# Performance work log

Hardware: AMD Instinct MI355X
Metric: run time of the kernel (lower is better)

## Reference

```python
import jax, jax.numpy as jnp
import numpy as np

N = 100000      # nodes
E = 1600000     # directed edges (avg degree 16)
F_IN = 256      # dataset.num_node_features
HID = 64        # hidden
C = 40          # dataset.num_classes


def setup_inputs() -> dict:
    key = jax.random.key(0)
    k0, k1, k2, k3 = jax.random.split(key, 4)
    x = jax.random.normal(k0, (N, F_IN), dtype=jnp.float32)
    edge_index = jax.random.randint(k1, (2, E), 0, N, dtype=jnp.int32)
    # Glorot-style init like GCNConv.reset_parameters
    W1 = jax.random.normal(k2, (F_IN, HID), dtype=jnp.float32) * (1.0 / np.sqrt(F_IN))
    b1 = jnp.zeros((HID,), dtype=jnp.float32)
    W2 = jax.random.normal(k3, (HID, C), dtype=jnp.float32) * (1.0 / np.sqrt(HID))
    b2 = jnp.zeros((C,), dtype=jnp.float32)
    return {"x": x, "edge_index": edge_index, "W1": W1, "b1": b1, "W2": W2, "b2": b2}


def gcn_conv(x, row, col, norm, W, b):
    # PyG GCNConv: out[col] += norm * (x @ W)[row]; then + bias
    n = x.shape[0]
    h = x @ W                                   # [N, out]
    msg = h[row] * norm[:, None]                # [E+N, out] gather + scale
    out = jax.ops.segment_sum(msg, col, num_segments=n)  # scatter-add
    return out + b


def _norm_coeffs(edge_index, n, dtype):
    # add self-loops, then symmetric normalization D^{-1/2} A D^{-1/2}
    loop = jnp.arange(n, dtype=edge_index.dtype)
    row = jnp.concatenate([edge_index[0], loop])
    col = jnp.concatenate([edge_index[1], loop])
    deg = jax.ops.segment_sum(jnp.ones_like(col, dtype=dtype), col, num_segments=n)
    dis = jnp.where(deg > 0, jax.lax.rsqrt(jnp.maximum(deg, 1.0)), 0.0)
    return row, col, dis[row] * dis[col]


def reference(x, edge_index, W1, b1, W2, b2):
    n = x.shape[0]
    row, col, norm = _norm_coeffs(edge_index, n, x.dtype)
    h = jax.nn.relu(gcn_conv(x, row, col, norm, W1, b1))
    # F.dropout(p=0.5, training=False) is identity in eval mode
    out = gcn_conv(h, row, col, norm, W2, b2)
    return jax.nn.log_softmax(out, axis=1)
```

## Files before the change

kernel.cpp:

```cpp
#include <hip/hip_runtime.h>
#include <math.h>

#define N_NODES 100000
#define N_EDGES 1600000
#define F_INDIM 256
#define HID 64
#define NCLS 40
#define NBKT 196
#define BKT_CAP 10240
#define EPB 8192

typedef __attribute__((ext_vector_type(8))) short short8;
typedef __attribute__((ext_vector_type(4))) float floatx4;

__device__ __forceinline__ unsigned short f2bf(float f) {
  unsigned u = __float_as_uint(f);
  unsigned r = (u + 0x7FFFu + ((u >> 16) & 1u)) >> 16;
  return (unsigned short)r;
}
__device__ __forceinline__ float bf2f(unsigned short h) {
  return __uint_as_float(((unsigned)h) << 16);
}
__device__ __forceinline__ void add8(float* a, uint4 u) {
  a[0] += __uint_as_float(u.x << 16);
  a[1] += __uint_as_float(u.x & 0xFFFF0000u);
  a[2] += __uint_as_float(u.y << 16);
  a[3] += __uint_as_float(u.y & 0xFFFF0000u);
  a[4] += __uint_as_float(u.z << 16);
  a[5] += __uint_as_float(u.z & 0xFFFF0000u);
  a[6] += __uint_as_float(u.w << 16);
  a[7] += __uint_as_float(u.w & 0xFFFF0000u);
}


__global__ __launch_bounds__(256) void k_zero(int* __restrict__ gcur,
                                              int* __restrict__ start) {
  int t = threadIdx.x;
  if (t < NBKT) gcur[t] = 0;
  if (t == 0) start[N_NODES] = N_EDGES;
}


__global__ __launch_bounds__(256) void k_binA(const int* __restrict__ row,
                                              const int* __restrict__ col,
                                              int* __restrict__ gcur,
                                              unsigned int* __restrict__ bktdata) {
  __shared__ int hist[NBKT];
  __shared__ int cur[NBKT];
  __shared__ int gbase[NBKT];
  const int t = threadIdx.x;
  const int e0 = blockIdx.x * EPB;
  const int n = min(EPB, N_EDGES - e0);
  if (t < NBKT) hist[t] = 0;
  __syncthreads();
  for (int i = t; i < n; i += 256) atomicAdd(&hist[col[e0 + i] >> 9], 1);
  __syncthreads();
  if (t < NBKT) {
    cur[t] = 0;
    int h = hist[t];
    gbase[t] = (h > 0) ? atomicAdd(&gcur[t], h) : 0;
  }
  __syncthreads();
  for (int i = t; i < n; i += 256) {
    int c = col[e0 + i];
    int r = row[e0 + i];
    int b = c >> 9;
    int p = atomicAdd(&cur[b], 1);
    bktdata[(size_t)b * BKT_CAP + gbase[b] + p] =
        ((unsigned)(c & 511) << 17) | (unsigned)r;
  }
}


__global__ __launch_bounds__(256) void k_histdis(const int* __restrict__ gcur,
                                                 const unsigned int* __restrict__ bktdata,
                                                 int* __restrict__ lscan,
                                                 float* __restrict__ dis) {
  __shared__ int h[512];
  const int b = blockIdx.x, t = threadIdx.x;
  h[t] = 0; h[t + 256] = 0;
  __syncthreads();
  const int cnt = gcur[b];
  const unsigned int* p = bktdata + (size_t)b * BKT_CAP;
  for (int i = t; i < cnt; i += 256) atomicAdd(&h[p[i] >> 17], 1);
  __syncthreads();
  const int n0 = b * 512 + t, n1 = n0 + 256;
  const int c0 = h[t], c1 = h[t + 256];
  if (n0 < N_NODES) dis[n0] = rsqrtf((float)(c0 + 1));
  if (n1 < N_NODES) dis[n1] = rsqrtf((float)(c1 + 1));
#pragma unroll
  for (int off = 1; off < 512; off <<= 1) {
    int u0 = (t >= off) ? h[t - off] : 0;
    int u1 = ((t + 256) >= off) ? h[t + 256 - off] : 0;
    __syncthreads();
    h[t] += u0; h[t + 256] += u1;
    __syncthreads();
  }
  if (n0 < N_NODES) lscan[n0] = h[t] - c0;
  if (n1 < N_NODES) lscan[n1] = h[t + 256] - c1;
}


__global__ __launch_bounds__(256) void k_scan2(const int* __restrict__ gcur,
                                               int* __restrict__ bsumS) {
  __shared__ int s[256];
  const int t = threadIdx.x;
  int v = (t < NBKT) ? gcur[t] : 0;
  s[t] = v;
  __syncthreads();
#pragma unroll
  for (int off = 1; off < 256; off <<= 1) {
    int u = (t >= off) ? s[t - off] : 0;
    __syncthreads();
    s[t] += u;
    __syncthreads();
  }
  if (t < NBKT) bsumS[t] = s[t] - v;
}


__global__ __launch_bounds__(256) void k_place(const int* __restrict__ gcur,
                                               const unsigned int* __restrict__ bktdata,
                                               const int* __restrict__ lscan,
                                               const int* __restrict__ bsumS,
                                               int* __restrict__ start,
                                               int* __restrict__ esrc) {
  __shared__ int cur[512];
  __shared__ int sbase[512];
  const int b = blockIdx.x, t = threadIdx.x;
  const int base = bsumS[b];
  const int n0 = b * 512 + t, n1 = n0 + 256;
  int s0 = ((n0 < N_NODES) ? lscan[n0] : 0) + base;
  int s1 = ((n1 < N_NODES) ? lscan[n1] : 0) + base;
  sbase[t] = s0; sbase[t + 256] = s1;
  if (n0 < N_NODES) start[n0] = s0;
  if (n1 < N_NODES) start[n1] = s1;
  cur[t] = 0; cur[t + 256] = 0;
  __syncthreads();
  const int cnt = gcur[b];
  const unsigned int* p = bktdata + (size_t)b * BKT_CAP;
  for (int i = t; i < cnt; i += 256) {
    unsigned u = p[i];
    int ld = u >> 17;
    int src = u & 0x1FFFF;
    int pos = sbase[ld] + atomicAdd(&cur[ld], 1);
    esrc[pos] = src;
  }
}


#define KP 264

__global__ __launch_bounds__(256) void k_gemm1(const float* __restrict__ x,
                                               const float* __restrict__ W1,
                                               const float* __restrict__ dis,
                                               unsigned short* __restrict__ h1b) {
  __shared__ unsigned short wt[HID * KP];
  const int tid = threadIdx.x;
  const int lane = tid & 63;
  const int w = tid >> 6;
  const int quad = lane >> 4;
  const int l15 = lane & 15;
  const int rowBase = blockIdx.x * 64;

#pragma unroll
  for (int i = 0; i < 16; ++i) {
    int f = tid + 256 * i;
    int k = f >> 4;
    int n0 = (f & 15) * 4;
    float4 v = *(const float4*)&W1[(size_t)k * HID + n0];
    wt[(n0 + 0) * KP + k] = f2bf(v.x);
    wt[(n0 + 1) * KP + k] = f2bf(v.y);
    wt[(n0 + 2) * KP + k] = f2bf(v.z);
    wt[(n0 + 3) * KP + k] = f2bf(v.w);
  }
  __syncthreads();

  const int ar = rowBase + w * 16 + l15;
  const float* xrow = x + (size_t)((ar < N_NODES) ? ar : N_NODES - 1) * F_INDIM + quad * 8;

  floatx4 acc[4];
#pragma unroll
  for (int c = 0; c < 4; ++c) acc[c] = (floatx4){0.f, 0.f, 0.f, 0.f};

#pragma unroll
  for (int kc = 0; kc < F_INDIM; kc += 32) {
    const float4 va = *(const float4*)(xrow + kc);
    const float4 vb = *(const float4*)(xrow + kc + 4);
    short8 a;
    a[0] = (short)f2bf(va.x); a[1] = (short)f2bf(va.y);
    a[2] = (short)f2bf(va.z); a[3] = (short)f2bf(va.w);
    a[4] = (short)f2bf(vb.x); a[5] = (short)f2bf(vb.y);
    a[6] = (short)f2bf(vb.z); a[7] = (short)f2bf(vb.w);
#pragma unroll
    for (int c = 0; c < 4; ++c) {
      const short8 b = *(const short8*)&wt[(c * 16 + l15) * KP + kc + quad * 8];
      acc[c] = __builtin_amdgcn_mfma_f32_16x16x32_bf16(a, b, acc[c], 0, 0, 0);
    }
  }

#pragma unroll
  for (int reg = 0; reg < 4; ++reg) {
    int gr = rowBase + w * 16 + quad * 4 + reg;
    if (gr < N_NODES) {
      float d = dis[gr];
#pragma unroll
      for (int c = 0; c < 4; ++c)
        h1b[(size_t)gr * HID + c * 16 + l15] = f2bf(d * acc[c][reg]);
    }
  }
}


__global__ __launch_bounds__(256) void k_agg1(const int* __restrict__ esrc,
                                              const int* __restrict__ start,
                                              const float* __restrict__ dis,
                                              const unsigned short* __restrict__ h1b,
                                              const float* __restrict__ b1,
                                              unsigned short* __restrict__ ab) {
  int gid = blockIdx.x * 256 + threadIdx.x;
  int node = gid >> 3;
  int q = gid & 7;
  if (node >= N_NODES) return;
  const uint4* hp4 = (const uint4*)h1b;
  int i = start[node];
  const int e1 = start[node + 1];
  float acc[8];
#pragma unroll
  for (int j = 0; j < 8; ++j) acc[j] = 0.f;
  for (; i + 2 <= e1; i += 2) {
    int s0 = esrc[i];
    int s1 = esrc[i + 1];
    uint4 u0 = hp4[(size_t)s0 * 8 + q];
    uint4 u1 = hp4[(size_t)s1 * 8 + q];
    add8(acc, u0);
    add8(acc, u1);
  }
  if (i < e1) {
    uint4 u = hp4[(size_t)esrc[i] * 8 + q];
    add8(acc, u);
  }
  uint4 us = hp4[(size_t)node * 8 + q];
  add8(acc, us);
  float d = dis[node];
  float4 ba = *(const float4*)&b1[q * 8];
  float4 bb = *(const float4*)&b1[q * 8 + 4];
  float v0 = fmaxf(d * acc[0] + ba.x, 0.f);
  float v1 = fmaxf(d * acc[1] + ba.y, 0.f);
  float v2 = fmaxf(d * acc[2] + ba.z, 0.f);
  float v3 = fmaxf(d * acc[3] + ba.w, 0.f);
  float v4 = fmaxf(d * acc[4] + bb.x, 0.f);
  float v5 = fmaxf(d * acc[5] + bb.y, 0.f);
  float v6 = fmaxf(d * acc[6] + bb.z, 0.f);
  float v7 = fmaxf(d * acc[7] + bb.w, 0.f);
  uint4 o;
  o.x = (unsigned)f2bf(v0) | ((unsigned)f2bf(v1) << 16);
  o.y = (unsigned)f2bf(v2) | ((unsigned)f2bf(v3) << 16);
  o.z = (unsigned)f2bf(v4) | ((unsigned)f2bf(v5) << 16);
  o.w = (unsigned)f2bf(v6) | ((unsigned)f2bf(v7) << 16);
  ((uint4*)ab)[(size_t)node * 8 + q] = o;
}


#define AP 72

__global__ __launch_bounds__(256) void k_gemm2(const unsigned short* __restrict__ ab,
                                               const float* __restrict__ W2,
                                               const float* __restrict__ dis,
                                               unsigned short* __restrict__ gb) {
  __shared__ unsigned short as[64 * AP];
  __shared__ unsigned short w2t[48 * AP];
  const int tid = threadIdx.x;
  const int lane = tid & 63;
  const int w = tid >> 6;
  const int quad = lane >> 4;
  const int l15 = lane & 15;
  const int rowBase = blockIdx.x * 64;

  for (int i = tid; i < 48 * 64; i += 256) {
    int n = i >> 6;
    int k = i & 63;
    w2t[n * AP + k] = (n < NCLS) ? f2bf(W2[(size_t)k * NCLS + n]) : (unsigned short)0;
  }
#pragma unroll
  for (int i = 0; i < 2; ++i) {
    int f = tid + 256 * i;
    int r = f >> 3;
    int q = f & 7;
    int gr = rowBase + r;
    short8 v = (short8){0, 0, 0, 0, 0, 0, 0, 0};
    if (gr < N_NODES) v = *(const short8*)&ab[(size_t)gr * HID + q * 8];
    *(short8*)&as[r * AP + q * 8] = v;
  }
  __syncthreads();

  floatx4 acc[3];
#pragma unroll
  for (int c = 0; c < 3; ++c) acc[c] = (floatx4){0.f, 0.f, 0.f, 0.f};

#pragma unroll
  for (int kh = 0; kh < 2; ++kh) {
    const short8 a = *(const short8*)&as[(w * 16 + l15) * AP + kh * 32 + quad * 8];
#pragma unroll
    for (int c = 0; c < 3; ++c) {
      const short8 b = *(const short8*)&w2t[(c * 16 + l15) * AP + kh * 32 + quad * 8];
      acc[c] = __builtin_amdgcn_mfma_f32_16x16x32_bf16(a, b, acc[c], 0, 0, 0);
    }
  }

#pragma unroll
  for (int reg = 0; reg < 4; ++reg) {
    int gr = rowBase + w * 16 + quad * 4 + reg;
    if (gr < N_NODES) {
      float d = dis[gr];
#pragma unroll
      for (int c = 0; c < 3; ++c) {
        int cc = c * 16 + l15;
        gb[(size_t)gr * 64 + cc] = f2bf(d * acc[c][reg]);
      }
      gb[(size_t)gr * 64 + 48 + l15] = 0;
    }
  }
}


__global__ __launch_bounds__(256) void k_agg2ls(const int* __restrict__ esrc,
                                                const int* __restrict__ start,
                                                const float* __restrict__ dis,
                                                const unsigned short* __restrict__ gb,
                                                const float* __restrict__ b2,
                                                float* __restrict__ out) {
  int gid = blockIdx.x * 256 + threadIdx.x;
  int node = gid >> 3;
  int q = gid & 7;
  if (node >= N_NODES) return;
  const uint4* gp4 = (const uint4*)gb;
  int i = start[node];
  const int e1 = start[node + 1];
  float acc[8];
#pragma unroll
  for (int j = 0; j < 8; ++j) acc[j] = 0.f;
  for (; i + 2 <= e1; i += 2) {
    int s0 = esrc[i];
    int s1 = esrc[i + 1];
    uint4 u0 = gp4[(size_t)s0 * 8 + q];
    uint4 u1 = gp4[(size_t)s1 * 8 + q];
    add8(acc, u0);
    add8(acc, u1);
  }
  if (i < e1) {
    uint4 u = gp4[(size_t)esrc[i] * 8 + q];
    add8(acc, u);
  }
  uint4 us = gp4[(size_t)node * 8 + q];
  add8(acc, us);
  const bool wr = q < 5;
  float v0 = 0.f, v1 = 0.f, v2 = 0.f, v3 = 0.f, v4 = 0.f, v5 = 0.f, v6 = 0.f, v7 = 0.f;
  float m = -INFINITY;
  if (wr) {
    float d = dis[node];
    float4 ba = *(const float4*)&b2[q * 8];
    float4 bb = *(const float4*)&b2[q * 8 + 4];
    v0 = d * acc[0] + ba.x;
    v1 = d * acc[1] + ba.y;
    v2 = d * acc[2] + ba.z;
    v3 = d * acc[3] + ba.w;
    v4 = d * acc[4] + bb.x;
    v5 = d * acc[5] + bb.y;
    v6 = d * acc[6] + bb.z;
    v7 = d * acc[7] + bb.w;
    m = fmaxf(fmaxf(fmaxf(v0, v1), fmaxf(v2, v3)),
              fmaxf(fmaxf(v4, v5), fmaxf(v6, v7)));
  }
#pragma unroll
  for (int off = 1; off < 8; off <<= 1) m = fmaxf(m, __shfl_xor(m, off));
  float el = 0.f;
  if (wr) {
    el = __expf(v0 - m) + __expf(v1 - m) + __expf(v2 - m) + __expf(v3 - m) +
         __expf(v4 - m) + __expf(v5 - m) + __expf(v6 - m) + __expf(v7 - m);
  }
#pragma unroll
  for (int off = 1; off < 8; off <<= 1) el += __shfl_xor(el, off);
  float ls = logf(el);
  if (wr) {
    float4 o1 = make_float4(v0 - m - ls, v1 - m - ls, v2 - m - ls, v3 - m - ls);
    float4 o2 = make_float4(v4 - m - ls, v5 - m - ls, v6 - m - ls, v7 - m - ls);
    *(float4*)&out[(size_t)node * NCLS + q * 8] = o1;
    *(float4*)&out[(size_t)node * NCLS + q * 8 + 4] = o2;
  }
}


extern "C" void kernel_launch(void* const* d_in, const int* in_sizes, int n_in,
                              void* d_out, int out_size, void* d_ws, size_t ws_size,
                              hipStream_t stream) {
  const float* x  = (const float*)d_in[0];
  const int*   ei = (const int*)d_in[1];
  const float* W1 = (const float*)d_in[2];
  const float* b1 = (const float*)d_in[3];
  const float* W2 = (const float*)d_in[4];
  const float* b2 = (const float*)d_in[5];
  float* out = (float*)d_out;

  const int* row = ei;
  const int* col = ei + N_EDGES;

  int*            esrc    = (int*)d_ws;
  unsigned int*   bktdata = (unsigned int*)(esrc + N_EDGES);
  unsigned short* h1b     = (unsigned short*)(bktdata + (size_t)NBKT * BKT_CAP);
  unsigned short* ab      = h1b + (size_t)N_NODES * HID;
  float*          dis     = (float*)(ab + (size_t)N_NODES * HID);
  int*            lscan   = (int*)(dis + N_NODES);
  int*            start   = lscan + N_NODES;
  int*            gcur    = start + N_NODES + 1;
  int*            bsumS   = gcur + NBKT;
  unsigned short* gb      = h1b;

  k_zero<<<1, 256, 0, stream>>>(gcur, start);
  k_binA<<<(N_EDGES + EPB - 1) / EPB, 256, 0, stream>>>(row, col, gcur, bktdata);
  k_histdis<<<NBKT, 256, 0, stream>>>(gcur, bktdata, lscan, dis);
  k_scan2<<<1, 256, 0, stream>>>(gcur, bsumS);
  k_place<<<NBKT, 256, 0, stream>>>(gcur, bktdata, lscan, bsumS, start, esrc);

  k_gemm1<<<(N_NODES + 63) / 64, 256, 0, stream>>>(x, W1, dis, h1b);
  k_agg1<<<(N_NODES * 8 + 255) / 256, 256, 0, stream>>>(esrc, start, dis, h1b, b1, ab);

  k_gemm2<<<(N_NODES + 63) / 64, 256, 0, stream>>>(ab, W2, dis, gb);
  k_agg2ls<<<(N_NODES * 8 + 255) / 256, 256, 0, stream>>>(esrc, start, dis, gb, b2, out);
}
```

Before: 325.2 us.

## Fuse CSR build histogram, scan and placement into one kernel; unroll gathers by four

The per-bucket histogram/dis kernel, the single-block bucket scan and the placement kernel are merged into one kernel. Each block now computes its own bucket base offset by reducing the counts of the preceding buckets with wave shuffles. This removes two launches and the lscan/bsumS round trips through global memory. Separately, both aggregation kernels unroll the neighbour gather loop from 2 to 4 to put more loads in flight, at some cost in registers.

```diff
diff --git a/kernel.cpp b/kernel.cpp
--- a/kernel.cpp
+++ b/kernel.cpp
@@ -33,11 +33,9 @@
 }
 
 
-__global__ __launch_bounds__(256) void k_zero(int* __restrict__ gcur,
-                                              int* __restrict__ start) {
+__global__ __launch_bounds__(256) void k_zero(int* __restrict__ gcur) {
   int t = threadIdx.x;
   if (t < NBKT) gcur[t] = 0;
-  if (t == 0) start[N_NODES] = N_EDGES;
 }
 
 
@@ -72,18 +70,30 @@
 }
 
 
-__global__ __launch_bounds__(256) void k_histdis(const int* __restrict__ gcur,
-                                                 const unsigned int* __restrict__ bktdata,
-                                                 int* __restrict__ lscan,
-                                                 float* __restrict__ dis) {
+__global__ __launch_bounds__(256) void k_build2(const int* __restrict__ gcur,
+                                                const unsigned int* __restrict__ bktdata,
+                                                float* __restrict__ dis,
+                                                int* __restrict__ start,
+                                                int* __restrict__ esrc) {
   __shared__ int h[512];
+  __shared__ int cur[512];
+  __shared__ int sbase[512];
+  __shared__ int wsum[4];
   const int b = blockIdx.x, t = threadIdx.x;
-  h[t] = 0; h[t + 256] = 0;
-  __syncthreads();
+  h[t] = 0; h[t + 256] = 0; cur[t] = 0; cur[t + 256] = 0;
+  int pv = (t < b) ? gcur[t] : 0;
+#pragma unroll
+  for (int off = 1; off < 64; off <<= 1) pv += __shfl_xor(pv, off);
+  if ((t & 63) == 0) wsum[t >> 6] = pv;
+  if (b == 0 && t == 0) start[N_NODES] = N_EDGES;
+  __syncthreads();
+  const int base = wsum[0] + wsum[1] + wsum[2] + wsum[3];
+
   const int cnt = gcur[b];
   const unsigned int* p = bktdata + (size_t)b * BKT_CAP;
   for (int i = t; i < cnt; i += 256) atomicAdd(&h[p[i] >> 17], 1);
   __syncthreads();
+
   const int n0 = b * 512 + t, n1 = n0 + 256;
   const int c0 = h[t], c1 = h[t + 256];
   if (n0 < N_NODES) dis[n0] = rsqrtf((float)(c0 + 1));
@@ -96,49 +106,13 @@
     h[t] += u0; h[t + 256] += u1;
     __syncthreads();
   }
-  if (n0 < N_NODES) lscan[n0] = h[t] - c0;
-  if (n1 < N_NODES) lscan[n1] = h[t + 256] - c1;
-}
-
-
-__global__ __launch_bounds__(256) void k_scan2(const int* __restrict__ gcur,
-                                               int* __restrict__ bsumS) {
-  __shared__ int s[256];
-  const int t = threadIdx.x;
-  int v = (t < NBKT) ? gcur[t] : 0;
-  s[t] = v;
-  __syncthreads();
-#pragma unroll
-  for (int off = 1; off < 256; off <<= 1) {
-    int u = (t >= off) ? s[t - off] : 0;
-    __syncthreads();
-    s[t] += u;
-    __syncthreads();
-  }
-  if (t < NBKT) bsumS[t] = s[t] - v;
-}
-
-
-__global__ __launch_bounds__(256) void k_place(const int* __restrict__ gcur,
-                                               const unsigned int* __restrict__ bktdata,
-                                               const int* __restrict__ lscan,
-                                               const int* __restrict__ bsumS,
-                                               int* __restrict__ start,
-                                               int* __restrict__ esrc) {
-  __shared__ int cur[512];
-  __shared__ int sbase[512];
-  const int b = blockIdx.x, t = threadIdx.x;
-  const int base = bsumS[b];
-  const int n0 = b * 512 + t, n1 = n0 + 256;
-  int s0 = ((n0 < N_NODES) ? lscan[n0] : 0) + base;
-  int s1 = ((n1 < N_NODES) ? lscan[n1] : 0) + base;
-  sbase[t] = s0; sbase[t + 256] = s1;
-  if (n0 < N_NODES) start[n0] = s0;
-  if (n1 < N_NODES) start[n1] = s1;
-  cur[t] = 0; cur[t + 256] = 0;
-  __syncthreads();
-  const int cnt = gcur[b];
-  const unsigned int* p = bktdata + (size_t)b * BKT_CAP;
+  const int sb0 = base + h[t] - c0;
+  const int sb1 = base + h[t + 256] - c1;
+  sbase[t] = sb0; sbase[t + 256] = sb1;
+  if (n0 < N_NODES) start[n0] = sb0;
+  if (n1 < N_NODES) start[n1] = sb1;
+  __syncthreads();
+
   for (int i = t; i < cnt; i += 256) {
     unsigned u = p[i];
     int ld = u >> 17;
@@ -228,15 +202,21 @@
   float acc[8];
 #pragma unroll
   for (int j = 0; j < 8; ++j) acc[j] = 0.f;
-  for (; i + 2 <= e1; i += 2) {
+  for (; i + 4 <= e1; i += 4) {
     int s0 = esrc[i];
     int s1 = esrc[i + 1];
+    int s2 = esrc[i + 2];
+    int s3 = esrc[i + 3];
     uint4 u0 = hp4[(size_t)s0 * 8 + q];
     uint4 u1 = hp4[(size_t)s1 * 8 + q];
+    uint4 u2 = hp4[(size_t)s2 * 8 + q];
+    uint4 u3 = hp4[(size_t)s3 * 8 + q];
     add8(acc, u0);
     add8(acc, u1);
-  }
-  if (i < e1) {
+    add8(acc, u2);
+    add8(acc, u3);
+  }
+  for (; i < e1; ++i) {
     uint4 u = hp4[(size_t)esrc[i] * 8 + q];
     add8(acc, u);
   }
@@ -340,15 +320,21 @@
   float acc[8];
 #pragma unroll
   for (int j = 0; j < 8; ++j) acc[j] = 0.f;
-  for (; i + 2 <= e1; i += 2) {
+  for (; i + 4 <= e1; i += 4) {
     int s0 = esrc[i];
     int s1 = esrc[i + 1];
+    int s2 = esrc[i + 2];
+    int s3 = esrc[i + 3];
     uint4 u0 = gp4[(size_t)s0 * 8 + q];
     uint4 u1 = gp4[(size_t)s1 * 8 + q];
+    uint4 u2 = gp4[(size_t)s2 * 8 + q];
+    uint4 u3 = gp4[(size_t)s3 * 8 + q];
     add8(acc, u0);
     add8(acc, u1);
-  }
-  if (i < e1) {
+    add8(acc, u2);
+    add8(acc, u3);
+  }
+  for (; i < e1; ++i) {
     uint4 u = gp4[(size_t)esrc[i] * 8 + q];
     add8(acc, u);
   }
@@ -410,17 +396,13 @@
   unsigned short* h1b     = (unsigned short*)(bktdata + (size_t)NBKT * BKT_CAP);
   unsigned short* ab      = h1b + (size_t)N_NODES * HID;
   float*          dis     = (float*)(ab + (size_t)N_NODES * HID);
-  int*            lscan   = (int*)(dis + N_NODES);
-  int*            start   = lscan + N_NODES;
+  int*            start   = (int*)(dis + N_NODES);
   int*            gcur    = start + N_NODES + 1;
-  int*            bsumS   = gcur + NBKT;
   unsigned short* gb      = h1b;
 
-  k_zero<<<1, 256, 0, stream>>>(gcur, start);
+  k_zero<<<1, 256, 0, stream>>>(gcur);
   k_binA<<<(N_EDGES + EPB - 1) / EPB, 256, 0, stream>>>(row, col, gcur, bktdata);
-  k_histdis<<<NBKT, 256, 0, stream>>>(gcur, bktdata, lscan, dis);
-  k_scan2<<<1, 256, 0, stream>>>(gcur, bsumS);
-  k_place<<<NBKT, 256, 0, stream>>>(gcur, bktdata, lscan, bsumS, start, esrc);
+  k_build2<<<NBKT, 256, 0, stream>>>(gcur, bktdata, dis, start, esrc);
 
   k_gemm1<<<(N_NODES + 63) / 64, 256, 0, stream>>>(x, W1, dis, h1b);
   k_agg1<<<(N_NODES * 8 + 255) / 256, 256, 0, stream>>>(esrc, start, dis, h1b, b1, ab);
```

Result: faster. 316.3 us (-2.8%).
